# Kernel optimization log

Hardware: AMD Instinct MI355X
Metric: run time of the kernel (lower is better)

Reference implementation:

```python
import jax, jax.numpy as jnp
import numpy as np

N = 250000   # atoms
E = 500000   # directed bond edges
B = 10000    # molecules
IN = 39      # atom feature dim (in_channels)
H = 128      # hidden_channels
ED = 10      # edge_dim
NUM_TIMESTEPS = 2


def setup_inputs() -> dict:
    key = jax.random.key(0)
    ks = iter(jax.random.split(key, 40))
    p = lambda shape: jax.random.normal(next(ks), shape, dtype=jnp.float32) * 0.05
    inp = {}
    inp["x"] = jax.random.normal(next(ks), (N, IN), dtype=jnp.float32)
    inp["edge_attr"] = jax.random.normal(next(ks), (E, ED), dtype=jnp.float32)
    # lin1
    inp["W_lin1"] = p((H, IN)); inp["b_lin1"] = p((H,))
    # GATEConv
    inp["gate_W1"] = p((H, H + ED)); inp["gate_W2"] = p((H, H))
    inp["gate_att_l"] = p((H,)); inp["gate_att_r"] = p((H,)); inp["gate_bias"] = p((H,))
    # GRUCell after GATEConv
    inp["gru1_Wih"] = p((3 * H, H)); inp["gru1_Whh"] = p((3 * H, H))
    inp["gru1_bih"] = p((3 * H,)); inp["gru1_bhh"] = p((3 * H,))
    # atom GATConv (num_layers-1 == 1)
    inp["conv_W"] = p((H, H)); inp["conv_att_src"] = p((H,)); inp["conv_att_dst"] = p((H,)); inp["conv_bias"] = p((H,))
    inp["gru2_Wih"] = p((3 * H, H)); inp["gru2_Whh"] = p((3 * H, H))
    inp["gru2_bih"] = p((3 * H,)); inp["gru2_bhh"] = p((3 * H,))
    # mol GATConv (bipartite atoms -> molecules, shared lin)
    inp["mol_W"] = p((H, H)); inp["mol_att_src"] = p((H,)); inp["mol_att_dst"] = p((H,)); inp["mol_bias"] = p((H,))
    inp["grum_Wih"] = p((3 * H, H)); inp["grum_Whh"] = p((3 * H, H))
    inp["grum_bih"] = p((3 * H,)); inp["grum_bhh"] = p((3 * H,))
    # lin2 + head
    inp["W_lin2"] = p((H, H)); inp["b_lin2"] = p((H,))
    inp["W_head"] = p((1, H)); inp["b_head"] = p((1,))
    inp["edge_index"] = jax.random.randint(next(ks), (2, E), 0, N, dtype=jnp.int32)
    inp["batch"] = jnp.sort(jax.random.randint(next(ks), (N,), 0, B, dtype=jnp.int32))
    return inp


def _gru(xg, hg, Wih, Whh, bih, bhh):
    # torch.nn.GRUCell semantics
    gi = xg @ Wih.T + bih
    gh = hg @ Whh.T + bhh
    ir, iz, inn = jnp.split(gi, 3, axis=-1)
    hr, hz, hn = jnp.split(gh, 3, axis=-1)
    r = jax.nn.sigmoid(ir + hr)
    z = jax.nn.sigmoid(iz + hz)
    n = jnp.tanh(inn + r * hn)
    return (1.0 - z) * n + z * hg


def _seg_softmax(logits, seg, num):
    # PyG softmax over target-index segments (stable, +1e-16 denom)
    m = jax.ops.segment_max(logits, seg, num_segments=num)
    e = jnp.exp(logits - m[seg])
    s = jax.ops.segment_sum(e, seg, num_segments=num)
    return e / (s[seg] + 1e-16)


def reference(x, edge_attr, W_lin1, b_lin1, gate_W1, gate_W2, gate_att_l, gate_att_r, gate_bias,
              gru1_Wih, gru1_Whh, gru1_bih, gru1_bhh,
              conv_W, conv_att_src, conv_att_dst, conv_bias,
              gru2_Wih, gru2_Whh, gru2_bih, gru2_bhh,
              mol_W, mol_att_src, mol_att_dst, mol_bias,
              grum_Wih, grum_Whh, grum_bih, grum_bhh,
              W_lin2, b_lin2, W_head, b_head,
              edge_index, batch):
    lrelu = lambda v: jax.nn.leaky_relu(v, 0.01)
    src, dst = edge_index[0], edge_index[1]  # (j, i): messages flow j -> i
    # initial atom embedding
    x = lrelu(x @ W_lin1.T + b_lin1)
    # ---- GATEConv (edge-attr-aware attention, aggr='add') ----
    xj = x[src]                                                   # [E, H]
    he = lrelu(jnp.concatenate([xj, edge_attr], axis=-1) @ gate_W1.T)
    alpha = lrelu(he @ gate_att_l + x[dst] @ gate_att_r)          # [E]
    alpha = _seg_softmax(alpha, dst, N)
    h = jax.ops.segment_sum((xj @ gate_W2.T) * alpha[:, None], dst, num_segments=N) + gate_bias
    h = jax.nn.elu(h)
    x = jax.nn.relu(_gru(h, x, gru1_Wih, gru1_Whh, gru1_bih, gru1_bhh))
    # ---- atom GATConv (heads=1, neg_slope=0.01, no self loops) ----
    xl = x @ conv_W.T
    a = lrelu((xl * conv_att_src).sum(-1)[src] + (xl * conv_att_dst).sum(-1)[dst])
    a = _seg_softmax(a, dst, N)
    h = jax.ops.segment_sum(xl[src] * a[:, None], dst, num_segments=N) + conv_bias
    h = jax.nn.relu(h)
    x = jax.nn.relu(_gru(h, x, gru2_Wih, gru2_Whh, gru2_bih, gru2_bhh))
    # ---- attentive graph readout: bipartite GAT atoms -> molecules ----
    out = jax.nn.relu(jax.ops.segment_sum(x, batch, num_segments=B))  # [B, H]
    for _ in range(NUM_TIMESTEPS):
        xs = x @ mol_W.T                                          # src transform [N, H]
        od = out @ mol_W.T                                        # dst transform [B, H]
        a = lrelu((xs * mol_att_src).sum(-1) + ((od * mol_att_dst).sum(-1))[batch])
        a = _seg_softmax(a, batch, B)
        h = jax.ops.segment_sum(xs * a[:, None], batch, num_segments=B) + mol_bias
        h = jax.nn.elu(h)
        out = jax.nn.relu(_gru(h, out, grum_Wih, grum_Whh, grum_bih, grum_bhh))
    out = out @ W_lin2.T + b_lin2
    out = out @ W_head.T + b_head                                 # [B, 1]
    return out.squeeze(-1)                                        # [B]
```

## Files before the change

kernel.cpp:

```cpp
#include <hip/hip_runtime.h>
#include <hip/hip_bf16.h>
#include <type_traits>

typedef __hip_bfloat16 bf16;

constexpr int N_  = 250000;
constexpr int E_  = 500000;
constexpr int B_  = 10000;
constexpr int H_  = 128;

typedef short s8v __attribute__((ext_vector_type(8)));
typedef float f4v __attribute__((ext_vector_type(4)));

__device__ __forceinline__ float b2f(bf16 v){ return __bfloat162float(v); }
__device__ __forceinline__ bf16  f2b(float v){ return __float2bfloat16(v); }
__device__ __forceinline__ float lrelu_f(float v){ return v > 0.f ? v : 0.01f*v; }
__device__ __forceinline__ float sigmoid_f(float x){ return __builtin_amdgcn_rcpf(1.f+__expf(-x)); }
__device__ __forceinline__ float tanh_f(float x){ return 1.f - 2.f*__builtin_amdgcn_rcpf(__expf(2.f*x)+1.f); }
__device__ __forceinline__ float elu_f(float v){ return v > 0.f ? v : __expf(v)-1.f; }
__device__ __forceinline__ unsigned f2b_bits(float f){
  bf16 h=__float2bfloat16(f); unsigned short s; __builtin_memcpy(&s,&h,2); return (unsigned)s;
}
__device__ __forceinline__ void unp8(uint4 v, float* o){
  o[0]=__uint_as_float(v.x<<16); o[1]=__uint_as_float(v.x&0xffff0000u);
  o[2]=__uint_as_float(v.y<<16); o[3]=__uint_as_float(v.y&0xffff0000u);
  o[4]=__uint_as_float(v.z<<16); o[5]=__uint_as_float(v.z&0xffff0000u);
  o[6]=__uint_as_float(v.w<<16); o[7]=__uint_as_float(v.w&0xffff0000u);
}

struct W2B { const float* s; bf16* d; int rows, ld, ow, cw; };
struct W2B9 { W2B seg[9]; };
__global__ void w2ball_k(W2B9 p){
  W2B g=p.seg[blockIdx.y];
  int i=blockIdx.x*256+threadIdx.x;
  if (i>=g.rows*g.ow) return;
  int r=i/g.ow, k=i-r*g.ow;
  g.d[i] = f2b(k<g.cw ? g.s[(size_t)r*g.ld+k] : 0.f);
}

__global__ __launch_bounds__(256) void lin1_mfma_k(const float* __restrict__ X0, const bf16* __restrict__ Wb,
                            const float* __restrict__ bias, const float* __restrict__ dvec,
                            bf16* __restrict__ Y, float* __restrict__ dout, int M){
  __shared__ __align__(16) bf16 sx[64][72];
  __shared__ float sdot[4][64];
  int wv=threadIdx.x>>6, lane=threadIdx.x&63;
  int n=lane&15, q=lane>>4;
  int c0=wv*32;
  s8v wB[2][2];
  #pragma unroll
  for (int ct=0;ct<2;ct++)
    #pragma unroll
    for (int kk=0;kk<2;kk++)
      wB[ct][kk]=*(const s8v*)(Wb+(size_t)(c0+ct*16+n)*64+kk*32+q*8);
  float bb[2];
  #pragma unroll
  for (int ct=0;ct<2;ct++) bb[ct]=bias[c0+ct*16+n];
  float va[2]={dvec[c0+n], dvec[c0+16+n]};
  for (int i=threadIdx.x;i<64*25;i+=256){ int r=i/25,k=39+(i-(i/25)*25); sx[r][k]=f2b(0.f); }
  for (long r0=(long)blockIdx.x*64; r0<M; r0+=(long)gridDim.x*64){
    __syncthreads();
    for (int f=threadIdx.x; f<64*39; f+=256){
      int r=f/39, k=f-(f/39)*39; long row=r0+r;
      sx[r][k]= f2b(row<M ? X0[row*39+k] : 0.f);
    }
    __syncthreads();
    s8v a[4][2];
    #pragma unroll
    for (int rt=0;rt<4;rt++)
      #pragma unroll
      for (int kk=0;kk<2;kk++)
        a[rt][kk]=*(const s8v*)&sx[rt*16+n][kk*32+q*8];
    f4v acc[4][2];
    #pragma unroll
    for (int rt=0;rt<4;rt++)
      #pragma unroll
      for (int ct=0;ct<2;ct++) acc[rt][ct]=(f4v){0.f,0.f,0.f,0.f};
    #pragma unroll
    for (int kk=0;kk<2;kk++)
      #pragma unroll
      for (int rt=0;rt<4;rt++)
        #pragma unroll
        for (int ct=0;ct<2;ct++)
          acc[rt][ct]=__builtin_amdgcn_mfma_f32_16x16x32_bf16(a[rt][kk],wB[ct][kk],acc[rt][ct],0,0,0);
    #pragma unroll
    for (int rt=0;rt<4;rt++){
      #pragma unroll
      for (int rg=0;rg<4;rg++){
        float y0=lrelu_f(acc[rt][0][rg]+bb[0]);
        float y1=lrelu_f(acc[rt][1][rg]+bb[1]);
        long row=r0+rt*16+q*4+rg;
        if (row<M){
          Y[row*128+c0+n]   =f2b(y0);
          Y[row*128+c0+16+n]=f2b(y1);
        }
        float pa=y0*va[0]+y1*va[1];
        #pragma unroll
        for (int o=1;o<16;o<<=1) pa+=__shfl_xor(pa,o);
        if (n==0) sdot[wv][rt*16+q*4+rg]=pa;
      }
    }
    __syncthreads();
    if (threadIdx.x<64){
      long row=r0+threadIdx.x;
      if (row<M) dout[row]=sdot[0][threadIdx.x]+sdot[1][threadIdx.x]+sdot[2][threadIdx.x]+sdot[3][threadIdx.x];
    }
  }
}

template<int ACT,int NDOT>
__global__ __launch_bounds__(256) void lin_mfma_k(const bf16* __restrict__ X, const bf16* __restrict__ Wb,
                            const float* __restrict__ bias, bf16* __restrict__ Y,
                            const float* __restrict__ v1, const float* __restrict__ v2,
                            float* __restrict__ d1, float* __restrict__ d2, int M){
  __shared__ float sdot[2][4][64];
  int wv=threadIdx.x>>6, lane=threadIdx.x&63;
  int n=lane&15, q=lane>>4;
  int c0=wv*32;
  s8v wB[2][4];
  #pragma unroll
  for (int ct=0;ct<2;ct++)
    #pragma unroll
    for (int kk=0;kk<4;kk++)
      wB[ct][kk]=*(const s8v*)(Wb+(size_t)(c0+ct*16+n)*128+kk*32+q*8);
  float bb[2];
  #pragma unroll
  for (int ct=0;ct<2;ct++) bb[ct]=bias? bias[c0+ct*16+n]:0.f;
  float va[2][2];
  if constexpr (NDOT>=1){ va[0][0]=v1[c0+n]; va[0][1]=v1[c0+16+n]; }
  if constexpr (NDOT>=2){ va[1][0]=v2[c0+n]; va[1][1]=v2[c0+16+n]; }
  for (long r0=(long)blockIdx.x*64; r0<M; r0+=(long)gridDim.x*64){
    s8v a[4][4];
    #pragma unroll
    for (int rt=0;rt<4;rt++){
      long row=r0+rt*16+n; if (row>=M) row=M-1;
      #pragma unroll
      for (int kk=0;kk<4;kk++) a[rt][kk]=*(const s8v*)(X+row*128+kk*32+q*8);
    }
    f4v acc[4][2];
    #pragma unroll
    for (int rt=0;rt<4;rt++)
      #pragma unroll
      for (int ct=0;ct<2;ct++) acc[rt][ct]=(f4v){0.f,0.f,0.f,0.f};
    #pragma unroll
    for (int kk=0;kk<4;kk++)
      #pragma unroll
      for (int rt=0;rt<4;rt++)
        #pragma unroll
        for (int ct=0;ct<2;ct++)
          acc[rt][ct]=__builtin_amdgcn_mfma_f32_16x16x32_bf16(a[rt][kk],wB[ct][kk],acc[rt][ct],0,0,0);
    #pragma unroll
    for (int rt=0;rt<4;rt++){
      #pragma unroll
      for (int rg=0;rg<4;rg++){
        float y0=acc[rt][0][rg]+bb[0];
        float y1=acc[rt][1][rg]+bb[1];
        if (ACT==2){ y0=elu_f(y0); y1=elu_f(y1); }
        long row=r0+rt*16+q*4+rg;
        if (row<M){
          Y[row*128+c0+n]   =f2b(y0);
          Y[row*128+c0+16+n]=f2b(y1);
        }
        if constexpr (NDOT>=1){
          float pa=y0*va[0][0]+y1*va[0][1];
          float pb=0.f;
          if constexpr (NDOT>=2) pb=y0*va[1][0]+y1*va[1][1];
          #pragma unroll
          for (int o=1;o<16;o<<=1){
            pa+=__shfl_xor(pa,o);
            if constexpr (NDOT>=2) pb+=__shfl_xor(pb,o);
          }
          if (n==0){
            sdot[0][wv][rt*16+q*4+rg]=pa;
            if constexpr (NDOT>=2) sdot[1][wv][rt*16+q*4+rg]=pb;
          }
        }
      }
    }
    if constexpr (NDOT>=1){
      __syncthreads();
      if (threadIdx.x<64){
        long row=r0+threadIdx.x;
        if (row<M){
          d1[row]=sdot[0][0][threadIdx.x]+sdot[0][1][threadIdx.x]+sdot[0][2][threadIdx.x]+sdot[0][3][threadIdx.x];
          if constexpr (NDOT>=2)
            d2[row]=sdot[1][0][threadIdx.x]+sdot[1][1][threadIdx.x]+sdot[1][2][threadIdx.x]+sdot[1][3][threadIdx.x];
        }
      }
      __syncthreads();
    }
  }
}

__global__ __launch_bounds__(512,1) void gru_mfma_k(const bf16* __restrict__ A, const bf16* __restrict__ X,
                            const bf16* __restrict__ Wih, const bf16* __restrict__ Whh,
                            const float* __restrict__ bih, const float* __restrict__ bhh,
                            bf16* __restrict__ dest, int M){
  __shared__ __align__(16) bf16 sA[2][32][136];
  __shared__ __align__(16) bf16 sX[2][32][136];
  int wv=threadIdx.x>>6, lane=threadIdx.x&63;
  int n=lane&15, q=lane>>4;
  int c0=wv*16;
  s8v wI[3][4], wH[3][4];
  #pragma unroll
  for (int g=0;g<3;g++)
    #pragma unroll
    for (int kk=0;kk<4;kk++){
      size_t off=((size_t)(g*128+c0+n))*128+kk*32+q*8;
      wI[g][kk]=*(const s8v*)(Wih+off);
      wH[g][kk]=*(const s8v*)(Whh+off);
    }
  int col=c0+n;
  float br =bih[col]+bhh[col];
  float bz =bih[128+col]+bhh[128+col];
  float bni=bih[256+col], bnh=bhh[256+col];

  int srow=wv*4+q;
  int schunk=n;
  long step=(long)gridDim.x*32;
  long r0=(long)blockIdx.x*32;
  int buf=0;
  {
    long rowg=r0+srow; if (rowg>=M) rowg=M-1;
    uint4 va=*(const uint4*)(A+rowg*128+schunk*8);
    uint4 vx=*(const uint4*)(X+rowg*128+schunk*8);
    *(uint4*)&sA[0][srow][schunk*8]=va;
    *(uint4*)&sX[0][srow][schunk*8]=vx;
  }
  __syncthreads();
  for (; r0<M; r0+=step){
    long rn=r0+step;
    uint4 va, vx; bool pre = rn<M;
    if (pre){
      long rowg=rn+srow; if (rowg>=M) rowg=M-1;
      va=*(const uint4*)(A+rowg*128+schunk*8);
      vx=*(const uint4*)(X+rowg*128+schunk*8);
    }
    f4v acc[6][2];
    #pragma unroll
    for (int g=0;g<6;g++)
      #pragma unroll
      for (int rt=0;rt<2;rt++) acc[g][rt]=(f4v){0.f,0.f,0.f,0.f};
    #pragma unroll
    for (int kk=0;kk<4;kk++){
      s8v aA[2], aX[2];
      #pragma unroll
      for (int rt=0;rt<2;rt++){
        aA[rt]=*(const s8v*)&sA[buf][rt*16+n][(kk*4+q)*8];
        aX[rt]=*(const s8v*)&sX[buf][rt*16+n][(kk*4+q)*8];
      }
      #pragma unroll
      for (int g=0;g<3;g++)
        #pragma unroll
        for (int rt=0;rt<2;rt++){
          acc[g  ][rt]=__builtin_amdgcn_mfma_f32_16x16x32_bf16(aA[rt],wI[g][kk],acc[g  ][rt],0,0,0);
          acc[3+g][rt]=__builtin_amdgcn_mfma_f32_16x16x32_bf16(aX[rt],wH[g][kk],acc[3+g][rt],0,0,0);
        }
    }
    float xv[2][4];
    #pragma unroll
    for (int rt=0;rt<2;rt++)
      #pragma unroll
      for (int rg=0;rg<4;rg++)
        xv[rt][rg]=b2f(sX[buf][rt*16+q*4+rg][col]);
    #pragma unroll
    for (int rt=0;rt<2;rt++){
      #pragma unroll
      for (int rg=0;rg<4;rg++){
        long row=r0+rt*16+q*4+rg;
        if (row<M){
          float rgate=sigmoid_f(acc[0][rt][rg]+acc[3][rt][rg]+br);
          float zgate=sigmoid_f(acc[1][rt][rg]+acc[4][rt][rg]+bz);
          float nn=tanh_f(acc[2][rt][rg]+bni + rgate*(acc[5][rt][rg]+bnh));
          float o=(1.f-zgate)*nn + zgate*xv[rt][rg];
          dest[row*128+col]=f2b(fmaxf(o,0.f));
        }
      }
    }
    if (pre){
      *(uint4*)&sA[buf^1][srow][schunk*8]=va;
      *(uint4*)&sX[buf^1][srow][schunk*8]=vx;
    }
    __syncthreads();
    buf^=1;
  }
}

__global__ __launch_bounds__(256) void gru_scalar_k(const float* __restrict__ A, const float* __restrict__ X,
                            const float* __restrict__ Wih, const float* __restrict__ Whh,
                            const float* __restrict__ bih, const float* __restrict__ bhh,
                            float* __restrict__ dest, int M){
  __shared__ unsigned sW[6][32*66];
  __shared__ float sA[8][132], sX[8][132];
  __shared__ float sbi[3][32], sbh[3][32];
  int c0 = blockIdx.y*32;
  for (int i=threadIdx.x; i<6*32*64; i+=256){
    int m=i>>11, r=i&2047, c=r>>6, k2=r&63;
    const float* base = (m<3)? Wih : Whh;
    int g = (m<3)? m : m-3;
    const float* wp = base + ((size_t)(g*128 + c0 + c))*128 + 2*k2;
    sW[m][c*66 + k2] = f2b_bits(wp[0]) | (f2b_bits(wp[1])<<16);
  }
  if (threadIdx.x < 96){
    int g=threadIdx.x>>5, c=threadIdx.x&31;
    sbi[g][c]=bih[g*128+c0+c]; sbh[g][c]=bhh[g*128+c0+c];
  }
  __syncthreads();
  int sub=threadIdx.x>>5, c=threadIdx.x&31;
  for (long r0=(long)blockIdx.x*8; r0<M; r0+=(long)gridDim.x*8){
    __syncthreads();
    for (int i=threadIdx.x;i<8*16;i+=256){
      int rr=i>>4, q=i&15; long row=r0+rr;
      if (row<M){
        *(float4*)&sA[rr][q*8]   = *(const float4*)(A+row*128+q*8);
        *(float4*)&sA[rr][q*8+4] = *(const float4*)(A+row*128+q*8+4);
        *(float4*)&sX[rr][q*8]   = *(const float4*)(X+row*128+q*8);
        *(float4*)&sX[rr][q*8+4] = *(const float4*)(X+row*128+q*8+4);
      } else {
        float4 z=make_float4(0,0,0,0);
        *(float4*)&sA[rr][q*8]=z; *(float4*)&sA[rr][q*8+4]=z;
        *(float4*)&sX[rr][q*8]=z; *(float4*)&sX[rr][q*8+4]=z;
      }
    }
    __syncthreads();
    long row=r0+sub;
    if (row<M){
      const unsigned* wri=&sW[0][c*66]; const unsigned* wzi=&sW[1][c*66]; const unsigned* wni=&sW[2][c*66];
      const unsigned* wrh=&sW[3][c*66]; const unsigned* wzh=&sW[4][c*66]; const unsigned* wnh=&sW[5][c*66];
      const float2* xa=(const float2*)sA[sub]; const float2* xb=(const float2*)sX[sub];
      float ari=0,azi=0,ani=0,arh=0,azh=0,anh=0;
      #pragma unroll 8
      for (int k2=0;k2<64;k2++){
        float2 av=xa[k2], bv=xb[k2];
        unsigned u;
        u=wri[k2]; ari += av.x*__uint_as_float(u<<16) + av.y*__uint_as_float(u&0xffff0000u);
        u=wzi[k2]; azi += av.x*__uint_as_float(u<<16) + av.y*__uint_as_float(u&0xffff0000u);
        u=wni[k2]; ani += av.x*__uint_as_float(u<<16) + av.y*__uint_as_float(u&0xffff0000u);
        u=wrh[k2]; arh += bv.x*__uint_as_float(u<<16) + bv.y*__uint_as_float(u&0xffff0000u);
        u=wzh[k2]; azh += bv.x*__uint_as_float(u<<16) + bv.y*__uint_as_float(u&0xffff0000u);
        u=wnh[k2]; anh += bv.x*__uint_as_float(u<<16) + bv.y*__uint_as_float(u&0xffff0000u);
      }
      float rg = sigmoid_f(ari+arh+sbi[0][c]+sbh[0][c]);
      float zg = sigmoid_f(azi+azh+sbi[1][c]+sbh[1][c]);
      float nn = tanh_f(ani+sbi[2][c] + rg*(anh+sbh[2][c]));
      float xv = sX[sub][c0+c];
      float o  = (1.f-zg)*nn + zg*xv;
      dest[row*128+c0+c] = fmaxf(o,0.f);
    }
  }
}

__global__ __launch_bounds__(256) void gate_edge_logits_k(const bf16* __restrict__ u, const float* __restrict__ ea,
                                   const float* __restrict__ gW1, const float* __restrict__ att_l,
                                   const float* __restrict__ ddst, const int* __restrict__ src,
                                   const int* __restrict__ dst, const int* __restrict__ epos,
                                   float* __restrict__ elog, int E){
  int wv=threadIdx.x>>6, lane=threadIdx.x&63;
  int t=lane&31;
  float w[10][4];
  #pragma unroll
  for (int k=0;k<10;k++)
    #pragma unroll
    for (int j=0;j<4;j++)
      w[k][j]=gW1[(size_t)(t*4+j)*138 + 128 + k];
  float al[4];
  #pragma unroll
  for (int j=0;j<4;j++) al[j]=att_l[t*4+j];

  long stride=(long)gridDim.x*8;
  long e=(long)blockIdx.x*8 + wv*2 + (lane>>5);
  if (e>=E) return;
  uint2 uv0,uv1; float2 ca0,cb0,cc0,cd0,ce0, ca1,cb1,cc1,cd1,ce1;
  float dv0=0.f,dv1=0.f; int ep0=0,ep1=0;
  {
    int sj=src[e];
    uv0=*(const uint2*)(u+(size_t)sj*128+t*4);
    const float2* er=(const float2*)(ea+(size_t)e*10);
    ca0=er[0]; cb0=er[1]; cc0=er[2]; cd0=er[3]; ce0=er[4];
    dv0=ddst[dst[e]]; ep0=epos[e];
  }
  long e1i=e+stride; bool h1=e1i<E;
  if (h1){
    int sj=src[e1i];
    uv1=*(const uint2*)(u+(size_t)sj*128+t*4);
    const float2* er=(const float2*)(ea+(size_t)e1i*10);
    ca1=er[0]; cb1=er[1]; cc1=er[2]; cd1=er[3]; ce1=er[4];
    dv1=ddst[dst[e1i]]; ep1=epos[e1i];
  }
  while (true){
    long e2i=e1i+stride; bool h2=e2i<E;
    uint2 uv2=make_uint2(0,0);
    float2 ca2={0,0},cb2={0,0},cc2={0,0},cd2={0,0},ce2={0,0};
    float dv2=0.f; int ep2=0;
    if (h2){
      int sj=src[e2i];
      uv2=*(const uint2*)(u+(size_t)sj*128+t*4);
      const float2* er=(const float2*)(ea+(size_t)e2i*10);
      ca2=er[0]; cb2=er[1]; cc2=er[2]; cd2=er[3]; ce2=er[4];
      dv2=ddst[dst[e2i]]; ep2=epos[e2i];
    }
    float uf[4];
    uf[0]=__uint_as_float(uv0.x<<16); uf[1]=__uint_as_float(uv0.x&0xffff0000u);
    uf[2]=__uint_as_float(uv0.y<<16); uf[3]=__uint_as_float(uv0.y&0xffff0000u);
    float acc=0.f;
    #pragma unroll
    for (int j=0;j<4;j++){
      float v=uf[j];
      v+=ca0.x*w[0][j]; v+=ca0.y*w[1][j];
      v+=cb0.x*w[2][j]; v+=cb0.y*w[3][j];
      v+=cc0.x*w[4][j]; v+=cc0.y*w[5][j];
      v+=cd0.x*w[6][j]; v+=cd0.y*w[7][j];
      v+=ce0.x*w[8][j]; v+=ce0.y*w[9][j];
      acc+=lrelu_f(v)*al[j];
    }
    #pragma unroll
    for (int o=16;o;o>>=1) acc+=__shfl_xor(acc,o);
    if (t==0) elog[ep0]=lrelu_f(acc+dv0);
    if (!h1) break;
    uv0=uv1; ca0=ca1; cb0=cb1; cc0=cc1; cd0=cd1; ce0=ce1; dv0=dv1; ep0=ep1;
    uv1=uv2; ca1=ca2; cb1=cb2; cc1=cc2; cd1=cd2; ce1=ce2; dv1=dv2; ep1=ep2;
    e1i=e2i; h1=h2;
  }
}

template<int ACT>
__global__ void node_gather_k(const float* __restrict__ elog, const int* __restrict__ srcp,
                              const int* __restrict__ ptr, const bf16* __restrict__ V,
                              const float* __restrict__ bias, bf16* __restrict__ S, int M){
  int wv=threadIdx.x>>6, lane=threadIdx.x&63;
  int g=lane>>4, t=lane&15;
  int node=blockIdx.x*16 + wv*4 + g;
  if (node>=M) return;
  int p0=ptr[node], p1=ptr[node+1];
  float m=-INFINITY;
  for (int p=p0+t;p<p1;p+=16) m=fmaxf(m,elog[p]);
  #pragma unroll
  for (int o=8;o;o>>=1) m=fmaxf(m,__shfl_xor(m,o));
  float ssum=0.f;
  float acc[8]={0,0,0,0,0,0,0,0};
  if (p0<p1){
    float lg=elog[p0];
    uint4 v=*(const uint4*)(V+(size_t)srcp[p0]*128+t*8);
    for (int p=p0+1;p<p1;p++){
      float lgn=elog[p];
      uint4 vn=*(const uint4*)(V+(size_t)srcp[p]*128+t*8);
      float e=__expf(lg-m); ssum+=e;
      float xf[8]; unp8(v,xf);
      #pragma unroll
      for (int j=0;j<8;j++) acc[j]+=e*xf[j];
      lg=lgn; v=vn;
    }
    float e=__expf(lg-m); ssum+=e;
    float xf[8]; unp8(v,xf);
    #pragma unroll
    for (int j=0;j<8;j++) acc[j]+=e*xf[j];
  }
  float inv=1.f/(ssum+1e-16f);
  #pragma unroll
  for (int j=0;j<8;j++) acc[j]*=inv;
  if (ACT==1){
    #pragma unroll
    for (int j=0;j<8;j++) acc[j]=fmaxf(acc[j]+bias[t*8+j],0.f);
  }
  uint4 o;
  o.x=f2b_bits(acc[0])|(f2b_bits(acc[1])<<16);
  o.y=f2b_bits(acc[2])|(f2b_bits(acc[3])<<16);
  o.z=f2b_bits(acc[4])|(f2b_bits(acc[5])<<16);
  o.w=f2b_bits(acc[6])|(f2b_bits(acc[7])<<16);
  *(uint4*)(S+(size_t)node*128+t*8)=o;
}

__global__ __launch_bounds__(256) void conv_gather_k(const float* __restrict__ dsrc, const float* __restrict__ ddst,
    const int* __restrict__ ptr, const int* __restrict__ srcp,
    const bf16* __restrict__ V, const float* __restrict__ bias, bf16* __restrict__ S, int M){
  int wv=threadIdx.x>>6, lane=threadIdx.x&63;
  int g=lane>>4, t=lane&15;
  int node=blockIdx.x*16 + wv*4 + g;
  if (node>=M) return;
  int p0=ptr[node], p1=ptr[node+1];
  float dvn=ddst[node];
  float m=-INFINITY, s=0.f;
  float acc[8]={0,0,0,0,0,0,0,0};
  if (p0<p1){
    int sj=srcp[p0];
    float ls=dsrc[sj];
    uint4 v=*(const uint4*)(V+(size_t)sj*128+t*8);
    for (int p=p0+1;p<p1;p++){
      int sjn=srcp[p];
      float lsn=dsrc[sjn];
      uint4 vn=*(const uint4*)(V+(size_t)sjn*128+t*8);
      float l=lrelu_f(ls+dvn);
      float mn=fmaxf(m,l), sc=__expf(m-mn), ee=__expf(l-mn);
      float xf[8]; unp8(v,xf);
      s=s*sc+ee;
      #pragma unroll
      for (int j=0;j<8;j++) acc[j]=acc[j]*sc+ee*xf[j];
      m=mn; ls=lsn; v=vn;
    }
    float l=lrelu_f(ls+dvn);
    float mn=fmaxf(m,l), sc=__expf(m-mn), ee=__expf(l-mn);
    float xf[8]; unp8(v,xf);
    s=s*sc+ee;
    #pragma unroll
    for (int j=0;j<8;j++) acc[j]=acc[j]*sc+ee*xf[j];
  }
  float inv=1.f/(s+1e-16f);
  uint4 o;
  float r0=fmaxf(acc[0]*inv+bias[t*8+0],0.f), r1=fmaxf(acc[1]*inv+bias[t*8+1],0.f);
  float r2=fmaxf(acc[2]*inv+bias[t*8+2],0.f), r3=fmaxf(acc[3]*inv+bias[t*8+3],0.f);
  float r4=fmaxf(acc[4]*inv+bias[t*8+4],0.f), r5=fmaxf(acc[5]*inv+bias[t*8+5],0.f);
  float r6=fmaxf(acc[6]*inv+bias[t*8+6],0.f), r7=fmaxf(acc[7]*inv+bias[t*8+7],0.f);
  o.x=f2b_bits(r0)|(f2b_bits(r1)<<16);
  o.y=f2b_bits(r2)|(f2b_bits(r3)<<16);
  o.z=f2b_bits(r4)|(f2b_bits(r5)<<16);
  o.w=f2b_bits(r6)|(f2b_bits(r7)<<16);
  *(uint4*)(S+(size_t)node*128+t*8)=o;
}

__global__ void mol_ptr_k(const int* __restrict__ batch, int* __restrict__ mptr, int n, int Bn){
  int b=blockIdx.x*256+threadIdx.x; if (b>Bn) return;
  if (b==Bn){ mptr[Bn]=n; return; }
  int lo=0, hi=n;
  while (lo<hi){ int mid=(lo+hi)>>1; if (batch[mid]<b) lo=mid+1; else hi=mid; }
  mptr[b]=lo;
}

__global__ void mol_sum_k(const bf16* __restrict__ x, const int* __restrict__ mptr,
                          float* __restrict__ out, int Bn){
  int wv=threadIdx.x>>6, lane=threadIdx.x&63;
  int b=blockIdx.x*4+wv; if (b>=Bn) return;
  int p0=mptr[b], p1=mptr[b+1];
  float a0=0.f,a1=0.f;
  for (int i=p0;i<p1;i++){ a0+=b2f(x[(size_t)i*128+lane]); a1+=b2f(x[(size_t)i*128+64+lane]); }
  out[(size_t)b*128+lane]=fmaxf(a0,0.f); out[(size_t)b*128+64+lane]=fmaxf(a1,0.f);
}

__global__ void fold_att_k(const float* __restrict__ W, const float* __restrict__ att,
                           float* __restrict__ wdd){
  int k=threadIdx.x; float a=0.f;
  for (int c=0;c<128;c++) a+=att[c]*W[(size_t)c*128+k];
  wdd[k]=a;
}

__global__ __launch_bounds__(256) void mol_fused_k(const float* __restrict__ dsrc, const int* __restrict__ mptr,
    const bf16* __restrict__ xs, const float* __restrict__ wdd, const float* __restrict__ outc,
    const float* __restrict__ bias, float* __restrict__ hb, int Bn){
  int wv=threadIdx.x>>6, lane=threadIdx.x&63;
  long b=(long)blockIdx.x*4+wv; if (b>=Bn) return;
  int p0=mptr[b], p1=mptr[b+1];
  float dd=outc[(size_t)b*128+lane]*wdd[lane]+outc[(size_t)b*128+64+lane]*wdd[64+lane];
  #pragma unroll
  for (int o=32;o;o>>=1) dd+=__shfl_xor(dd,o);
  float m=-INFINITY, s=0.f, a0=0.f, a1=0.f;
  for (int i=p0;i<p1;i++){
    float a=lrelu_f(dsrc[i]+dd);
    float x0=b2f(xs[(size_t)i*128+lane]), x1=b2f(xs[(size_t)i*128+64+lane]);
    float mn=fmaxf(m,a), sc=__expf(m-mn), ee=__expf(a-mn);
    s=s*sc+ee; a0=a0*sc+ee*x0; a1=a1*sc+ee*x1; m=mn;
  }
  float inv=1.f/(s+1e-16f);
  hb[(size_t)b*128+lane]=elu_f(a0*inv+bias[lane]);
  hb[(size_t)b*128+64+lane]=elu_f(a1*inv+bias[64+lane]);
}

__global__ void fold_head_k(const float* __restrict__ W2, const float* __restrict__ b2,
                            const float* __restrict__ Wh, const float* __restrict__ bh,
                            float* __restrict__ v){
  __shared__ float sred[128];
  int k=threadIdx.x;
  float a=0.f;
  for (int c=0;c<128;c++) a+=Wh[c]*W2[(size_t)c*128+k];
  v[k]=a;
  sred[k]=b2[k]*Wh[k]; __syncthreads();
  for (int o=64;o;o>>=1){ if (k<o) sred[k]+=sred[k+o]; __syncthreads(); }
  if (k==0) v[128]=sred[0]+bh[0];
}

__global__ void head_dot_k(const float* __restrict__ out, const float* __restrict__ v,
                           float* __restrict__ y, int M){
  __shared__ float sv[129];
  if (threadIdx.x<129) sv[threadIdx.x]=v[threadIdx.x];
  __syncthreads();
  int wv=threadIdx.x>>6, lane=threadIdx.x&63;
  long row=(long)blockIdx.x*4+wv;
  if (row>=M) return;
  float a=out[row*128+lane]*sv[lane]+out[row*128+64+lane]*sv[64+lane];
  #pragma unroll
  for (int o=32;o;o>>=1) a+=__shfl_xor(a,o);
  if (!lane) y[row]=a+sv[128];
}

__global__ void zero_i32_k(int* p, int n){ int i=blockIdx.x*256+threadIdx.x; if (i<n) p[i]=0; }
__global__ void hist_k(const int* __restrict__ dst, int* __restrict__ deg, int n){
  int e=blockIdx.x*256+threadIdx.x; if (e<n) atomicAdd(&deg[dst[e]],1);
}
__global__ void scan1_k(const int* __restrict__ deg, int* __restrict__ ptr,
                        int* __restrict__ part, int n){
  __shared__ int sd[256];
  int base=blockIdx.x*1024, tid=threadIdx.x;
  int v[4]; int ssum=0;
  #pragma unroll
  for (int j=0;j<4;j++){ int idx=base+tid*4+j; v[j]= idx<n? deg[idx]:0; ssum+=v[j]; }
  sd[tid]=ssum; __syncthreads();
  for (int o=1;o<256;o<<=1){ int t = tid>=o? sd[tid-o]:0; __syncthreads(); sd[tid]+=t; __syncthreads(); }
  int excl=sd[tid]-ssum;
  #pragma unroll
  for (int j=0;j<4;j++){ int idx=base+tid*4+j; if (idx<n) ptr[idx]=excl; excl+=v[j]; }
  if (tid==255) part[blockIdx.x]=sd[255];
}
__global__ void scan2_k(int* part, int nb){
  __shared__ int sd[512];
  int tid=threadIdx.x;
  int v= tid<nb? part[tid]:0; sd[tid]=v; __syncthreads();
  for (int o=1;o<512;o<<=1){ int t = tid>=o? sd[tid-o]:0; __syncthreads(); sd[tid]+=t; __syncthreads(); }
  if (tid<nb) part[tid]=sd[tid]-v;
}
__global__ void scan3_k(int* __restrict__ ptr, const int* __restrict__ part,
                        int* __restrict__ wofs, int n, int total){
  int i=blockIdx.x*256+threadIdx.x;
  if (i<n){ int val=ptr[i]+part[i>>10]; ptr[i]=val; wofs[i]=val; }
  if (i==0) ptr[n]=total;
}
__global__ void fill_csr_k(const int* __restrict__ dst, const int* __restrict__ src,
                           int* __restrict__ wofs, int* __restrict__ srcp,
                           int* __restrict__ epos, int n){
  int e=blockIdx.x*256+threadIdx.x;
  if (e<n){ int p=atomicAdd(&wofs[dst[e]],1); srcp[p]=src[e]; epos[e]=p; }
}

extern "C" void kernel_launch(void* const* d_in, const int* in_sizes, int n_in,
                              void* d_out, int out_size, void* d_ws, size_t ws_size,
                              hipStream_t stream){
  (void)in_sizes; (void)n_in; (void)out_size; (void)ws_size;
  const float* x0        =(const float*)d_in[0];
  const float* edge_attr =(const float*)d_in[1];
  const float* W_lin1    =(const float*)d_in[2];
  const float* b_lin1    =(const float*)d_in[3];
  const float* gate_W1   =(const float*)d_in[4];
  const float* gate_W2   =(const float*)d_in[5];
  const float* gate_att_l=(const float*)d_in[6];
  const float* gate_att_r=(const float*)d_in[7];
  const float* gate_bias =(const float*)d_in[8];
  const float* g1_Wih=(const float*)d_in[9];  const float* g1_Whh=(const float*)d_in[10];
  const float* g1_bih=(const float*)d_in[11]; const float* g1_bhh=(const float*)d_in[12];
  const float* conv_W=(const float*)d_in[13];
  const float* conv_att_src=(const float*)d_in[14];
  const float* conv_att_dst=(const float*)d_in[15];
  const float* conv_bias   =(const float*)d_in[16];
  const float* g2_Wih=(const float*)d_in[17]; const float* g2_Whh=(const float*)d_in[18];
  const float* g2_bih=(const float*)d_in[19]; const float* g2_bhh=(const float*)d_in[20];
  const float* mol_W=(const float*)d_in[21];
  const float* mol_att_src=(const float*)d_in[22];
  const float* mol_att_dst=(const float*)d_in[23];
  const float* mol_bias   =(const float*)d_in[24];
  const float* gm_Wih=(const float*)d_in[25]; const float* gm_Whh=(const float*)d_in[26];
  const float* gm_bih=(const float*)d_in[27]; const float* gm_bhh=(const float*)d_in[28];
  const float* W_lin2=(const float*)d_in[29]; const float* b_lin2=(const float*)d_in[30];
  const float* W_head=(const float*)d_in[31]; const float* b_head=(const float*)d_in[32];
  const int* ei   =(const int*)d_in[33];
  const int* batch=(const int*)d_in[34];
  const int* src=ei; const int* dst=ei+E_;
  float* y=(float*)d_out;

  const size_t NH=(size_t)N_*H_, BH=(size_t)B_*H_;
  bf16* b0  =(bf16*)d_ws;
  bf16* b1  =b0+NH;
  bf16* b2v =b1+NH;
  float* outA=(float*)(b2v+NH);
  float* outB=outA+BH;
  float* hb  =outB+BH;
  float* elog=hb+BH;
  float* dsrc=elog+E_;
  float* ddst=dsrc+N_;
  float* alog=ddst+N_;
  float* wdd =alog+N_;
  float* dd  =wdd+128;
  int* deg =(int*)(dd+B_);
  int* ptr =deg+N_;
  int* wofs=ptr+N_+1;
  int* part=wofs+N_;
  int* mptr=part+512;
  int* srcp=mptr+B_+1;
  int* epos=srcp+E_;
  uintptr_t wbase=((uintptr_t)(epos+E_)+255)&~(uintptr_t)255;
  bf16* wb_gw1 =(bf16*)wbase;
  bf16* wb_gw2 =wb_gw1 +128*128;
  bf16* wb_conv=wb_gw2 +128*128;
  bf16* wb_mol =wb_conv+128*128;
  bf16* wb_g1i =wb_mol +128*128;
  bf16* wb_g1h =wb_g1i +384*128;
  bf16* wb_g2i =wb_g1h +384*128;
  bf16* wb_g2h =wb_g2i +384*128;
  bf16* wb_l1  =wb_g2h +384*128;

  W2B9 wp;
  wp.seg[0]={gate_W1,wb_gw1,128,138,128,128};
  wp.seg[1]={gate_W2,wb_gw2,128,128,128,128};
  wp.seg[2]={conv_W ,wb_conv,128,128,128,128};
  wp.seg[3]={mol_W  ,wb_mol ,128,128,128,128};
  wp.seg[4]={g1_Wih,wb_g1i,384,128,128,128};
  wp.seg[5]={g1_Whh,wb_g1h,384,128,128,128};
  wp.seg[6]={g2_Wih,wb_g2i,384,128,128,128};
  wp.seg[7]={g2_Whh,wb_g2h,384,128,128,128};
  wp.seg[8]={W_lin1,wb_l1 ,128, 39, 64, 39};
  w2ball_k<<<dim3(192,9),256,0,stream>>>(wp);

  zero_i32_k<<<(N_+255)/256,256,0,stream>>>(deg,N_);
  hist_k<<<(E_+255)/256,256,0,stream>>>(dst,deg,E_);
  int nb=(N_+1023)/1024;
  scan1_k<<<nb,256,0,stream>>>(deg,ptr,part,N_);
  scan2_k<<<1,512,0,stream>>>(part,nb);
  scan3_k<<<(N_+255)/256,256,0,stream>>>(ptr,part,wofs,N_,E_);
  fill_csr_k<<<(E_+255)/256,256,0,stream>>>(dst,src,wofs,srcp,epos,E_);
  mol_ptr_k<<<(B_+1+255)/256,256,0,stream>>>(batch,mptr,N_,B_);

  lin1_mfma_k<<<1024,256,0,stream>>>(x0,wb_l1,b_lin1,gate_att_r,b0,ddst,N_);

  const int GL=768, GN=(N_+15)/16;
  lin_mfma_k<0,0><<<GL,256,0,stream>>>(b0,wb_gw1,nullptr,b1,nullptr,nullptr,nullptr,nullptr,N_);
  gate_edge_logits_k<<<8192,256,0,stream>>>(b1,edge_attr,gate_W1,gate_att_l,ddst,src,dst,epos,elog,E_);
  node_gather_k<0><<<GN,256,0,stream>>>(elog,srcp,ptr,b0,nullptr,b2v,N_);
  lin_mfma_k<2,0><<<GL,256,0,stream>>>(b2v,wb_gw2,gate_bias,b1,nullptr,nullptr,nullptr,nullptr,N_);
  gru_mfma_k<<<1024,512,0,stream>>>(b1,b0,wb_g1i,wb_g1h,g1_bih,g1_bhh,b2v,N_);
  lin_mfma_k<0,2><<<GL,256,0,stream>>>(b2v,wb_conv,nullptr,b0,conv_att_src,conv_att_dst,dsrc,ddst,N_);
  conv_gather_k<<<GN,256,0,stream>>>(dsrc,ddst,ptr,srcp,b0,conv_bias,b1,N_);
  gru_mfma_k<<<1024,512,0,stream>>>(b1,b2v,wb_g2i,wb_g2h,g2_bih,g2_bhh,b0,N_);
  mol_sum_k<<<(B_+3)/4,256,0,stream>>>(b0,mptr,outA,B_);
  lin_mfma_k<0,1><<<GL,256,0,stream>>>(b0,wb_mol,nullptr,b1,mol_att_src,nullptr,dsrc,nullptr,N_);
  fold_att_k<<<1,128,0,stream>>>(mol_W,mol_att_dst,wdd);
  float* out_cur=outA; float* out_nxt=outB;
  dim3 gm(157,4);
  for (int ts=0; ts<2; ts++){
    mol_fused_k<<<(B_+3)/4,256,0,stream>>>(dsrc,mptr,b1,wdd,out_cur,mol_bias,hb,B_);
    gru_scalar_k<<<gm,256,0,stream>>>(hb,out_cur,gm_Wih,gm_Whh,gm_bih,gm_bhh,out_nxt,B_);
    float* tmp=out_cur; out_cur=out_nxt; out_nxt=tmp;
  }
  fold_head_k<<<1,128,0,stream>>>(W_lin2,b_lin2,W_head,b_head,elog);
  head_dot_k<<<(B_+3)/4,256,0,stream>>>(out_cur,elog,y,B_);
}
```

Baseline: 1.072 ms.

## Fuse gate W2 linear into GRU kernel and process gate edges in source order

The separate gate_W2 linear kernel is removed. Its MFMA matmul, bias and ELU now run inside a new GRU kernel that stages the result in shared memory, so one write and re-read of the N×128 intermediate no longer goes through global memory. The gate edge-logit kernel now walks edges sorted by source node, built with a second histogram/scan/fill pass, so reads of node features are grouped by source. In exchange, edge-attribute reads and logit writes become scattered, and several extra preprocessing launches are added. The software pipeline in that kernel also drops from two stages of prefetch to one.

Measured after the change: 1.123 ms. 1.05x slower.

```diff
diff --git a/kernel.cpp b/kernel.cpp
--- a/kernel.cpp
+++ b/kernel.cpp
@@ -285,6 +285,122 @@
   }
 }
 
+__global__ __launch_bounds__(512,1) void gru_gw2_mfma_k(const bf16* __restrict__ S, const bf16* __restrict__ X,
+                            const bf16* __restrict__ Wg, const float* __restrict__ gbias,
+                            const bf16* __restrict__ Wih, const bf16* __restrict__ Whh,
+                            const float* __restrict__ bih, const float* __restrict__ bhh,
+                            bf16* __restrict__ dest, int M){
+  __shared__ __align__(16) bf16 sS[2][32][136];
+  __shared__ __align__(16) bf16 sX[2][32][136];
+  __shared__ __align__(16) bf16 sA[32][136];
+  int wv=threadIdx.x>>6, lane=threadIdx.x&63;
+  int n=lane&15, q=lane>>4;
+  int c0=wv*16;
+  s8v wI[3][4], wH[3][4], wG[4];
+  #pragma unroll
+  for (int g=0;g<3;g++)
+    #pragma unroll
+    for (int kk=0;kk<4;kk++){
+      size_t off=((size_t)(g*128+c0+n))*128+kk*32+q*8;
+      wI[g][kk]=*(const s8v*)(Wih+off);
+      wH[g][kk]=*(const s8v*)(Whh+off);
+    }
+  #pragma unroll
+  for (int kk=0;kk<4;kk++)
+    wG[kk]=*(const s8v*)(Wg+(size_t)(c0+n)*128+kk*32+q*8);
+  int col=c0+n;
+  float bA =gbias[col];
+  float br =bih[col]+bhh[col];
+  float bz =bih[128+col]+bhh[128+col];
+  float bni=bih[256+col], bnh=bhh[256+col];
+
+  int srow=wv*4+q;
+  int schunk=n;
+  long step=(long)gridDim.x*32;
+  long r0=(long)blockIdx.x*32;
+  int buf=0;
+  {
+    long rowg=r0+srow; if (rowg>=M) rowg=M-1;
+    uint4 vs=*(const uint4*)(S+rowg*128+schunk*8);
+    uint4 vx=*(const uint4*)(X+rowg*128+schunk*8);
+    *(uint4*)&sS[0][srow][schunk*8]=vs;
+    *(uint4*)&sX[0][srow][schunk*8]=vx;
+  }
+  __syncthreads();
+  for (; r0<M; r0+=step){
+    long rn=r0+step;
+    uint4 vs, vx; bool pre = rn<M;
+    if (pre){
+      long rowg=rn+srow; if (rowg>=M) rowg=M-1;
+      vs=*(const uint4*)(S+rowg*128+schunk*8);
+      vx=*(const uint4*)(X+rowg*128+schunk*8);
+    }
+    f4v accA[2];
+    accA[0]=(f4v){0.f,0.f,0.f,0.f}; accA[1]=(f4v){0.f,0.f,0.f,0.f};
+    #pragma unroll
+    for (int kk=0;kk<4;kk++){
+      #pragma unroll
+      for (int rt=0;rt<2;rt++){
+        s8v aS=*(const s8v*)&sS[buf][rt*16+n][(kk*4+q)*8];
+        accA[rt]=__builtin_amdgcn_mfma_f32_16x16x32_bf16(aS,wG[kk],accA[rt],0,0,0);
+      }
+    }
+    #pragma unroll
+    for (int rt=0;rt<2;rt++)
+      #pragma unroll
+      for (int rg=0;rg<4;rg++)
+        sA[rt*16+q*4+rg][col]=f2b(elu_f(accA[rt][rg]+bA));
+    __syncthreads();
+    f4v acc[6][2];
+    #pragma unroll
+    for (int g=0;g<6;g++)
+      #pragma unroll
+      for (int rt=0;rt<2;rt++) acc[g][rt]=(f4v){0.f,0.f,0.f,0.f};
+    #pragma unroll
+    for (int kk=0;kk<4;kk++){
+      s8v aA[2], aX[2];
+      #pragma unroll
+      for (int rt=0;rt<2;rt++){
+        aA[rt]=*(const s8v*)&sA[rt*16+n][(kk*4+q)*8];
+        aX[rt]=*(const s8v*)&sX[buf][rt*16+n][(kk*4+q)*8];
+      }
+      #pragma unroll
+      for (int g=0;g<3;g++)
+        #pragma unroll
+        for (int rt=0;rt<2;rt++){
+          acc[g  ][rt]=__builtin_amdgcn_mfma_f32_16x16x32_bf16(aA[rt],wI[g][kk],acc[g  ][rt],0,0,0);
+          acc[3+g][rt]=__builtin_amdgcn_mfma_f32_16x16x32_bf16(aX[rt],wH[g][kk],acc[3+g][rt],0,0,0);
+        }
+    }
+    float xv[2][4];
+    #pragma unroll
+    for (int rt=0;rt<2;rt++)
+      #pragma unroll
+      for (int rg=0;rg<4;rg++)
+        xv[rt][rg]=b2f(sX[buf][rt*16+q*4+rg][col]);
+    #pragma unroll
+    for (int rt=0;rt<2;rt++){
+      #pragma unroll
+      for (int rg=0;rg<4;rg++){
+        long row=r0+rt*16+q*4+rg;
+        if (row<M){
+          float rgate=sigmoid_f(acc[0][rt][rg]+acc[3][rt][rg]+br);
+          float zgate=sigmoid_f(acc[1][rt][rg]+acc[4][rt][rg]+bz);
+          float nn=tanh_f(acc[2][rt][rg]+bni + rgate*(acc[5][rt][rg]+bnh));
+          float o=(1.f-zgate)*nn + zgate*xv[rt][rg];
+          dest[row*128+col]=f2b(fmaxf(o,0.f));
+        }
+      }
+    }
+    if (pre){
+      *(uint4*)&sS[buf^1][srow][schunk*8]=vs;
+      *(uint4*)&sX[buf^1][srow][schunk*8]=vx;
+    }
+    __syncthreads();
+    buf^=1;
+  }
+}
+
 __global__ __launch_bounds__(256) void gru_scalar_k(const float* __restrict__ A, const float* __restrict__ X,
                             const float* __restrict__ Wih, const float* __restrict__ Whh,
                             const float* __restrict__ bih, const float* __restrict__ bhh,
@@ -349,11 +465,11 @@
   }
 }
 
-__global__ __launch_bounds__(256) void gate_edge_logits_k(const bf16* __restrict__ u, const float* __restrict__ ea,
+__global__ __launch_bounds__(256) void gate_edge_src_k(const bf16* __restrict__ u, const float* __restrict__ ea,
                                    const float* __restrict__ gW1, const float* __restrict__ att_l,
-                                   const float* __restrict__ ddst, const int* __restrict__ src,
-                                   const int* __restrict__ dst, const int* __restrict__ epos,
-                                   float* __restrict__ elog, int E){
+                                   const float* __restrict__ ddst, const int* __restrict__ sidx,
+                                   const int* __restrict__ sjarr, const int* __restrict__ dst,
+                                   const int* __restrict__ epos, float* __restrict__ elog, int E){
   int wv=threadIdx.x>>6, lane=threadIdx.x&63;
   int t=lane&31;
   float w[10][4];
@@ -367,58 +483,46 @@
   for (int j=0;j<4;j++) al[j]=att_l[t*4+j];
 
   long stride=(long)gridDim.x*8;
-  long e=(long)blockIdx.x*8 + wv*2 + (lane>>5);
-  if (e>=E) return;
-  uint2 uv0,uv1; float2 ca0,cb0,cc0,cd0,ce0, ca1,cb1,cc1,cd1,ce1;
-  float dv0=0.f,dv1=0.f; int ep0=0,ep1=0;
-  {
-    int sj=src[e];
-    uv0=*(const uint2*)(u+(size_t)sj*128+t*4);
-    const float2* er=(const float2*)(ea+(size_t)e*10);
-    ca0=er[0]; cb0=er[1]; cc0=er[2]; cd0=er[3]; ce0=er[4];
-    dv0=ddst[dst[e]]; ep0=epos[e];
-  }
-  long e1i=e+stride; bool h1=e1i<E;
-  if (h1){
-    int sj=src[e1i];
-    uv1=*(const uint2*)(u+(size_t)sj*128+t*4);
-    const float2* er=(const float2*)(ea+(size_t)e1i*10);
-    ca1=er[0]; cb1=er[1]; cc1=er[2]; cd1=er[3]; ce1=er[4];
-    dv1=ddst[dst[e1i]]; ep1=epos[e1i];
-  }
+  long p=(long)blockIdx.x*8 + wv*2 + (lane>>5);
+  if (p>=E) return;
+  int e=sidx[p], j0=sjarr[p];
+  uint2 uv=*(const uint2*)(u+(size_t)j0*128+t*4);
+  const float2* er=(const float2*)(ea+(size_t)e*10);
+  float2 c0=er[0],c1=er[1],c2=er[2],c3=er[3],c4=er[4];
+  float dv=ddst[dst[e]];
+  int ep=epos[e];
   while (true){
-    long e2i=e1i+stride; bool h2=e2i<E;
-    uint2 uv2=make_uint2(0,0);
-    float2 ca2={0,0},cb2={0,0},cc2={0,0},cd2={0,0},ce2={0,0};
-    float dv2=0.f; int ep2=0;
-    if (h2){
-      int sj=src[e2i];
-      uv2=*(const uint2*)(u+(size_t)sj*128+t*4);
-      const float2* er=(const float2*)(ea+(size_t)e2i*10);
-      ca2=er[0]; cb2=er[1]; cc2=er[2]; cd2=er[3]; ce2=er[4];
-      dv2=ddst[dst[e2i]]; ep2=epos[e2i];
+    long pn=p+stride; bool has=pn<E;
+    uint2 uvn=make_uint2(0,0);
+    float2 d0={0,0},d1={0,0},d2={0,0},d3={0,0},d4={0,0};
+    float dvn=0.f; int epn=0;
+    if (has){
+      int en=sidx[pn], jn=sjarr[pn];
+      uvn=*(const uint2*)(u+(size_t)jn*128+t*4);
+      const float2* ern=(const float2*)(ea+(size_t)en*10);
+      d0=ern[0];d1=ern[1];d2=ern[2];d3=ern[3];d4=ern[4];
+      dvn=ddst[dst[en]];
+      epn=epos[en];
     }
     float uf[4];
-    uf[0]=__uint_as_float(uv0.x<<16); uf[1]=__uint_as_float(uv0.x&0xffff0000u);
-    uf[2]=__uint_as_float(uv0.y<<16); uf[3]=__uint_as_float(uv0.y&0xffff0000u);
+    uf[0]=__uint_as_float(uv.x<<16); uf[1]=__uint_as_float(uv.x&0xffff0000u);
+    uf[2]=__uint_as_float(uv.y<<16); uf[3]=__uint_as_float(uv.y&0xffff0000u);
     float acc=0.f;
     #pragma unroll
     for (int j=0;j<4;j++){
       float v=uf[j];
-      v+=ca0.x*w[0][j]; v+=ca0.y*w[1][j];
-      v+=cb0.x*w[2][j]; v+=cb0.y*w[3][j];
-      v+=cc0.x*w[4][j]; v+=cc0.y*w[5][j];
-      v+=cd0.x*w[6][j]; v+=cd0.y*w[7][j];
-      v+=ce0.x*w[8][j]; v+=ce0.y*w[9][j];
+      v+=c0.x*w[0][j]; v+=c0.y*w[1][j];
+      v+=c1.x*w[2][j]; v+=c1.y*w[3][j];
+      v+=c2.x*w[4][j]; v+=c2.y*w[5][j];
+      v+=c3.x*w[6][j]; v+=c3.y*w[7][j];
+      v+=c4.x*w[8][j]; v+=c4.y*w[9][j];
       acc+=lrelu_f(v)*al[j];
     }
     #pragma unroll
     for (int o=16;o;o>>=1) acc+=__shfl_xor(acc,o);
-    if (t==0) elog[ep0]=lrelu_f(acc+dv0);
-    if (!h1) break;
-    uv0=uv1; ca0=ca1; cb0=cb1; cc0=cc1; cd0=cd1; ce0=ce1; dv0=dv1; ep0=ep1;
-    uv1=uv2; ca1=ca2; cb1=cb2; cc1=cc2; cd1=cd2; ce1=ce2; dv1=dv2; ep1=ep2;
-    e1i=e2i; h1=h2;
+    if (t==0) elog[ep]=lrelu_f(acc+dv);
+    if (!has) break;
+    p=pn; uv=uvn; c0=d0;c1=d1;c2=d2;c3=d3;c4=d4; dv=dvn; ep=epn;
   }
 }
 
@@ -625,6 +729,11 @@
                            int* __restrict__ epos, int n){
   int e=blockIdx.x*256+threadIdx.x;
   if (e<n){ int p=atomicAdd(&wofs[dst[e]],1); srcp[p]=src[e]; epos[e]=p; }
+}
+__global__ void fill_src_k(const int* __restrict__ src, int* __restrict__ wofsS,
+                           int* __restrict__ sidx, int* __restrict__ sjarr, int n){
+  int e=blockIdx.x*256+threadIdx.x;
+  if (e<n){ int j=src[e]; int p=atomicAdd(&wofsS[j],1); sidx[p]=e; sjarr[p]=j; }
 }
 
 extern "C" void kernel_launch(void* const* d_in, const int* in_sizes, int n_in,
@@ -691,6 +800,9 @@
   bf16* wb_g2i =wb_g1h +384*128;
   bf16* wb_g2h =wb_g2i +384*128;
   bf16* wb_l1  =wb_g2h +384*128;
+  int* ptrS =(int*)outB;
+  int* sidx =(int*)hb;
+  int* sjarr=sidx+E_;
 
   W2B9 wp;
   wp.seg[0]={gate_W1,wb_gw1,128,138,128,128};
@@ -704,23 +816,28 @@
   wp.seg[8]={W_lin1,wb_l1 ,128, 39, 64, 39};
   w2ball_k<<<dim3(192,9),256,0,stream>>>(wp);
 
+  int nb=(N_+1023)/1024;
   zero_i32_k<<<(N_+255)/256,256,0,stream>>>(deg,N_);
   hist_k<<<(E_+255)/256,256,0,stream>>>(dst,deg,E_);
-  int nb=(N_+1023)/1024;
   scan1_k<<<nb,256,0,stream>>>(deg,ptr,part,N_);
   scan2_k<<<1,512,0,stream>>>(part,nb);
   scan3_k<<<(N_+255)/256,256,0,stream>>>(ptr,part,wofs,N_,E_);
   fill_csr_k<<<(E_+255)/256,256,0,stream>>>(dst,src,wofs,srcp,epos,E_);
+  zero_i32_k<<<(N_+255)/256,256,0,stream>>>(deg,N_);
+  hist_k<<<(E_+255)/256,256,0,stream>>>(src,deg,E_);
+  scan1_k<<<nb,256,0,stream>>>(deg,ptrS,part,N_);
+  scan2_k<<<1,512,0,stream>>>(part,nb);
+  scan3_k<<<(N_+255)/256,256,0,stream>>>(ptrS,part,wofs,N_,E_);
+  fill_src_k<<<(E_+255)/256,256,0,stream>>>(src,wofs,sidx,sjarr,E_);
   mol_ptr_k<<<(B_+1+255)/256,256,0,stream>>>(batch,mptr,N_,B_);
 
   lin1_mfma_k<<<1024,256,0,stream>>>(x0,wb_l1,b_lin1,gate_att_r,b0,ddst,N_);
 
   const int GL=768, GN=(N_+15)/16;
   lin_mfma_k<0,0><<<GL,256,0,stream>>>(b0,wb_gw1,nullptr,b1,nullptr,nullptr,nullptr,nullptr,N_);
-  gate_edge_logits_k<<<8192,256,0,stream>>>(b1,edge_attr,gate_W1,gate_att_l,ddst,src,dst,epos,elog,E_);
+  gate_edge_src_k<<<8192,256,0,stream>>>(b1,edge_attr,gate_W1,gate_att_l,ddst,sidx,sjarr,dst,epos,elog,E_);
   node_gather_k<0><<<GN,256,0,stream>>>(elog,srcp,ptr,b0,nullptr,b2v,N_);
-  lin_mfma_k<2,0><<<GL,256,0,stream>>>(b2v,wb_gw2,gate_bias,b1,nullptr,nullptr,nullptr,nullptr,N_);
-  gru_mfma_k<<<1024,512,0,stream>>>(b1,b0,wb_g1i,wb_g1h,g1_bih,g1_bhh,b2v,N_);
+  gru_gw2_mfma_k<<<1024,512,0,stream>>>(b2v,b0,wb_gw2,gate_bias,wb_g1i,wb_g1h,g1_bih,g1_bhh,b2v,N_);
   lin_mfma_k<0,2><<<GL,256,0,stream>>>(b2v,wb_conv,nullptr,b0,conv_att_src,conv_att_dst,dsrc,ddst,N_);
   conv_gather_k<<<GN,256,0,stream>>>(dsrc,ddst,ptr,srcp,b0,conv_bias,b1,N_);
   gru_mfma_k<<<1024,512,0,stream>>>(b1,b2v,wb_g2i,wb_g2h,g2_bih,g2_bhh,b0,N_);
```
